# Kernel optimization log

Measured on AMD Instinct MI355X. Metric: run time of the kernel, lower is better.

## Reference

```python
import jax, jax.numpy as jnp
import numpy as np

N = 50000
E = 1600000
DIM = 128
RC = 5.0
DEPTH = 3


def setup_inputs() -> dict:
    key = jax.random.key(0)
    kv, ke, ks, kd, kw, kb, krs, ksig = jax.random.split(key, 8)
    v = jax.random.normal(kv, (N, DIM), dtype=jnp.float32)
    # edge distances in [0, rc]
    e = jax.random.uniform(ke, (E, 1), dtype=jnp.float32) * RC
    src = jax.random.randint(ks, (E,), 0, N, dtype=jnp.int32)
    dst = jax.random.randint(kd, (E,), 0, N, dtype=jnp.int32)
    # learned params: A = nn.Linear(dim, dim); rs, sigma = torch.rand(1)
    A_w = jax.random.normal(kw, (DIM, DIM), dtype=jnp.float32) / np.sqrt(DIM)
    A_b = jax.random.normal(kb, (DIM,), dtype=jnp.float32) * 0.01
    rs = jax.random.uniform(krs, (1,), dtype=jnp.float32)
    sigma = jax.random.uniform(ksig, (1,), dtype=jnp.float32)
    return {"v": v, "e": e, "src": src, "dst": dst,
            "A_w": A_w, "A_b": A_b, "rs": rs, "sigma": sigma}


def _edge_envelope(r, rs, sigma):
    # exp(-(r-rs)^2/sigma^2) * 0.5 * cos(pi*r/rc) * (r < rc)
    gauss = jnp.exp(-jnp.square(r - rs) / jnp.square(sigma))
    cutoff = 0.5 * jnp.cos(np.pi * r / RC) * (r < RC).astype(r.dtype)
    return gauss * cutoff


def reference(v, e, src, dst, A_w, A_b, rs, sigma):
    f = _edge_envelope(e, rs, sigma)  # [E, 1]
    cur = v
    for _ in range(DEPTH):
        msg = f * cur[src]  # gather src node feats, weight by edge envelope: [E, DIM]
        svf = jax.ops.segment_sum(msg, dst, num_segments=N)  # scatter-sum to dst: [N, DIM]
        cur = jax.nn.relu((svf + v) @ A_w.T + A_b)  # linear + relu, skip from original v
    return cur
```

## Files before the change

### kernel.cpp

```cpp
#include <hip/hip_runtime.h>
#include <math.h>

#define N_NODES 50000
#define N_PAD   50048
#define N_EDGES 1600000
#define DIM     128
#define RCUT    5.0f
#define NGROUP  (N_PAD / 64)
#define NB_PRE  512
#define CH_PRE  (N_EDGES / NB_PRE)
#define NB_CONV 6250
#define NB_WPREP 8
#define NB_SUB  8
#define B_SUB   (NB_PRE / NB_SUB)
#define XPAD    136
#define NTILE   (N_PAD / 16)

typedef __attribute__((ext_vector_type(8))) __bf16 bf16x8;
typedef __attribute__((ext_vector_type(4))) float  f32x4;

__device__ __forceinline__ float bf_lo(unsigned int u) { return __uint_as_float(u << 16); }
__device__ __forceinline__ float bf_hi(unsigned int u) { return __uint_as_float(u & 0xffff0000u); }
__device__ __forceinline__ unsigned short f2bf(float x) {
    unsigned int u = __float_as_uint(x);
    u += 0x7fffu + ((u >> 16) & 1u);
    return (unsigned short)(u >> 16);
}

__global__ __launch_bounds__(256) void preA_kernel(
        const float* __restrict__ v, unsigned short* __restrict__ vb,
        const float* __restrict__ Aw, uint4* __restrict__ wfrag,
        const int* __restrict__ dst, int* __restrict__ partial) {
    int b = blockIdx.x;
    if (b < NB_CONV) {
        int i = b * 256 + threadIdx.x;
        float4 x = ((const float4*)v)[i];
        uint2 o;
        o.x = (unsigned)f2bf(x.x) | ((unsigned)f2bf(x.y) << 16);
        o.y = (unsigned)f2bf(x.z) | ((unsigned)f2bf(x.w) << 16);
        ((uint2*)vb)[i] = o;
    } else if (b < NB_CONV + NB_WPREP) {
        int t = (b - NB_CONV) * 256 + threadIdx.x;
        int lane = t & 63, nt = (t >> 6) & 7, kk = t >> 9;
        int n  = nt * 16 + (lane & 15);
        int k0 = kk * 32 + (lane >> 4) * 8;
        unsigned short h[8];
        #pragma unroll
        for (int i = 0; i < 8; ++i) h[i] = f2bf(Aw[n * DIM + k0 + i]);
        uint4 o;
        o.x = h[0] | ((unsigned)h[1] << 16); o.y = h[2] | ((unsigned)h[3] << 16);
        o.z = h[4] | ((unsigned)h[5] << 16); o.w = h[6] | ((unsigned)h[7] << 16);
        wfrag[t] = o;
    } else {
        __shared__ int h[NGROUP];
        int cb = b - NB_CONV - NB_WPREP, tid = threadIdx.x;
        for (int g = tid; g < NGROUP; g += 256) h[g] = 0;
        __syncthreads();
        int beg = cb * CH_PRE, end = beg + CH_PRE;
        for (int i = beg + tid; i < end; i += 256)
            atomicAdd(&h[dst[i] >> 6], 1);
        __syncthreads();
        for (int g = tid; g < NGROUP; g += 256) partial[cb * NGROUP + g] = h[g];
    }
}

__global__ __launch_bounds__(256) void ktot2_kernel(const int* __restrict__ partial,
                                                    int* __restrict__ partial2) {
    int gb = blockIdx.x & 3, bb = blockIdx.x >> 2;
    int g = gb * 256 + threadIdx.x;
    if (g >= NGROUP) return;
    int s = 0;
    int b0 = bb * B_SUB;
    for (int b = b0; b < b0 + B_SUB; ++b) s += partial[b * NGROUP + g];
    partial2[bb * NGROUP + g] = s;
}

__global__ __launch_bounds__(256) void kscan_kernel(const int* __restrict__ partial2,
                                                    int* __restrict__ goff) {
    __shared__ int part[256];
    int tid = threadIdx.x;
    int i0 = tid * 4;
    int v[4]; int s = 0;
    #pragma unroll
    for (int k = 0; k < 4; ++k) {
        int i = i0 + k; int t = 0;
        if (i < NGROUP) {
            #pragma unroll
            for (int bb = 0; bb < NB_SUB; ++bb) t += partial2[bb * NGROUP + i];
        }
        v[k] = t; s += t;
    }
    part[tid] = s; __syncthreads();
    for (int d = 1; d < 256; d <<= 1) {
        int val = (tid >= d) ? part[tid - d] : 0;
        __syncthreads(); part[tid] += val; __syncthreads();
    }
    int run = (tid == 0) ? 0 : part[tid - 1];
    #pragma unroll
    for (int k = 0; k < 4; ++k) {
        int i = i0 + k;
        if (i < NGROUP) { goff[i] = run; run += v[k]; }
    }
    if (tid == 0) goff[NGROUP] = N_EDGES;
}

__global__ __launch_bounds__(256) void kbase2_kernel(const int* __restrict__ partial,
                                                     const int* __restrict__ partial2,
                                                     const int* __restrict__ goff,
                                                     int* __restrict__ pbase) {
    int gb = blockIdx.x & 3, bb = blockIdx.x >> 2;
    int g = gb * 256 + threadIdx.x;
    if (g >= NGROUP) return;
    int run = goff[g];
    for (int b2 = 0; b2 < bb; ++b2) run += partial2[b2 * NGROUP + g];
    int b0 = bb * B_SUB;
    for (int b = b0; b < b0 + B_SUB; ++b) {
        pbase[b * NGROUP + g] = run;
        run += partial[b * NGROUP + g];
    }
}

__global__ __launch_bounds__(512) void reorder_kernel(
        const float* __restrict__ e,
        const int*   __restrict__ src,
        const int*   __restrict__ dst,
        const float* __restrict__ rs,
        const float* __restrict__ sigma,
        const int*   __restrict__ pbase,
        int2* __restrict__ metaT) {
    __shared__ int base[NGROUP];
    __shared__ int cnt[NGROUP];
    int b = blockIdx.x, tid = threadIdx.x;
    for (int g = tid; g < NGROUP; g += 512) { base[g] = pbase[b * NGROUP + g]; cnt[g] = 0; }
    __syncthreads();
    float rsv = rs[0], sg = sigma[0];
    int beg = b * CH_PRE, end = beg + CH_PRE;
    for (int i = beg + tid; i < end; i += 512) {
        float r  = e[i];
        float d  = r - rsv;
        float gauss = expf(-(d * d) / (sg * sg));
        float cut   = 0.5f * cosf(r * (float)(M_PI / (double)RCUT));
        cut = (r < RCUT) ? cut : 0.0f;
        float fe = gauss * cut;
        int dn = dst[i];
        int g  = dn >> 6;
        int lr = atomicAdd(&cnt[g], 1);
        metaT[base[g] + lr] = make_int2(src[i] * (DIM * 2) | ((dn & 63) << 24),
                                        __float_as_int(fe));
    }
}

#define EDGE2(mx, mf, rr)                                        \
    do {                                                         \
        float ff = __int_as_float(mf);                           \
        a0 = fmaf(ff, bf_lo(rr), a0);                            \
        a1 = fmaf(ff, bf_hi(rr), a1);                            \
    } while (0)

__device__ __forceinline__ void gather_node(
        const int2* __restrict__ meta, const char* basec,
        int beg, int end, float& a0, float& a1) {
    int c = beg;
    if ((c & 1) && c < end) {
        int2 m = meta[c];
        unsigned rr = *(const unsigned*)(basec + (unsigned)m.x);
        EDGE2(m.x, m.y, rr);
        ++c;
    }
    for (; c + 16 <= end; c += 16) {
        int4 m0 = *(const int4*)(meta + c);
        int4 m1 = *(const int4*)(meta + c + 2);
        int4 m2 = *(const int4*)(meta + c + 4);
        int4 m3 = *(const int4*)(meta + c + 6);
        int4 m4 = *(const int4*)(meta + c + 8);
        int4 m5 = *(const int4*)(meta + c + 10);
        int4 m6 = *(const int4*)(meta + c + 12);
        int4 m7 = *(const int4*)(meta + c + 14);
        unsigned r0  = *(const unsigned*)(basec + (unsigned)m0.x);
        unsigned r1  = *(const unsigned*)(basec + (unsigned)m0.z);
        unsigned r2  = *(const unsigned*)(basec + (unsigned)m1.x);
        unsigned r3  = *(const unsigned*)(basec + (unsigned)m1.z);
        unsigned r4  = *(const unsigned*)(basec + (unsigned)m2.x);
        unsigned r5  = *(const unsigned*)(basec + (unsigned)m2.z);
        unsigned r6  = *(const unsigned*)(basec + (unsigned)m3.x);
        unsigned r7  = *(const unsigned*)(basec + (unsigned)m3.z);
        unsigned r8  = *(const unsigned*)(basec + (unsigned)m4.x);
        unsigned r9  = *(const unsigned*)(basec + (unsigned)m4.z);
        unsigned r10 = *(const unsigned*)(basec + (unsigned)m5.x);
        unsigned r11 = *(const unsigned*)(basec + (unsigned)m5.z);
        unsigned r12 = *(const unsigned*)(basec + (unsigned)m6.x);
        unsigned r13 = *(const unsigned*)(basec + (unsigned)m6.z);
        unsigned r14 = *(const unsigned*)(basec + (unsigned)m7.x);
        unsigned r15 = *(const unsigned*)(basec + (unsigned)m7.z);
        EDGE2(m0.x, m0.y, r0);  EDGE2(m0.z, m0.w, r1);
        EDGE2(m1.x, m1.y, r2);  EDGE2(m1.z, m1.w, r3);
        EDGE2(m2.x, m2.y, r4);  EDGE2(m2.z, m2.w, r5);
        EDGE2(m3.x, m3.y, r6);  EDGE2(m3.z, m3.w, r7);
        EDGE2(m4.x, m4.y, r8);  EDGE2(m4.z, m4.w, r9);
        EDGE2(m5.x, m5.y, r10); EDGE2(m5.z, m5.w, r11);
        EDGE2(m6.x, m6.y, r12); EDGE2(m6.z, m6.w, r13);
        EDGE2(m7.x, m7.y, r14); EDGE2(m7.z, m7.w, r15);
    }
    if (c + 8 <= end) {
        int4 m0 = *(const int4*)(meta + c);
        int4 m1 = *(const int4*)(meta + c + 2);
        int4 m2 = *(const int4*)(meta + c + 4);
        int4 m3 = *(const int4*)(meta + c + 6);
        unsigned r0 = *(const unsigned*)(basec + (unsigned)m0.x);
        unsigned r1 = *(const unsigned*)(basec + (unsigned)m0.z);
        unsigned r2 = *(const unsigned*)(basec + (unsigned)m1.x);
        unsigned r3 = *(const unsigned*)(basec + (unsigned)m1.z);
        unsigned r4 = *(const unsigned*)(basec + (unsigned)m2.x);
        unsigned r5 = *(const unsigned*)(basec + (unsigned)m2.z);
        unsigned r6 = *(const unsigned*)(basec + (unsigned)m3.x);
        unsigned r7 = *(const unsigned*)(basec + (unsigned)m3.z);
        EDGE2(m0.x, m0.y, r0); EDGE2(m0.z, m0.w, r1);
        EDGE2(m1.x, m1.y, r2); EDGE2(m1.z, m1.w, r3);
        EDGE2(m2.x, m2.y, r4); EDGE2(m2.z, m2.w, r5);
        EDGE2(m3.x, m3.y, r6); EDGE2(m3.z, m3.w, r7);
        c += 8;
    }
    for (; c < end; ++c) {
        int2 m = meta[c];
        unsigned rr = *(const unsigned*)(basec + (unsigned)m.x);
        EDGE2(m.x, m.y, rr);
    }
}

__global__ __launch_bounds__(512) void layer0_kernel(
        const unsigned short* __restrict__ cur,
        const unsigned short* __restrict__ vb,
        const int2*  __restrict__ metaT,
        const int*   __restrict__ goff,
        int2* __restrict__ meta,
        int*  __restrict__ off,
        const uint4* __restrict__ wfrag,
        const float* __restrict__ bias,
        unsigned short* __restrict__ out_bf) {
    __shared__ unsigned short xlds[64 * XPAD];
    __shared__ int c64[64], b64[65], cu64[64];
    int tid = threadIdx.x;
    int wv  = tid >> 6, lane = tid & 63;
    int g   = blockIdx.x;
    int sbeg = goff[g], send = goff[g + 1];

    if (tid < 64) c64[tid] = 0;
    __syncthreads();
    for (int i = sbeg + tid; i < send; i += 512)
        atomicAdd(&c64[(metaT[i].x >> 24) & 63], 1);
    __syncthreads();
    if (tid == 0) {
        int run = 0;
        #pragma unroll
        for (int t = 0; t < 64; ++t) { b64[t] = run; cu64[t] = run; run += c64[t]; }
        b64[64] = run;
    }
    __syncthreads();
    if (tid < 64) {
        int node = g * 64 + tid;
        if (node <= N_NODES) off[node] = sbeg + b64[tid];
    }
    for (int i = sbeg + tid; i < send; i += 512) {
        int2 m = metaT[i];
        int tag = (m.x >> 24) & 63;
        int lr = atomicAdd(&cu64[tag], 1);
        meta[sbeg + lr] = make_int2(m.x & 0x00FFFFFF, m.y);
    }
    __syncthreads();

    int n0 = g * 64 + wv * 8;
    int myoff = 0;
    if (lane < 9) myoff = sbeg + b64[wv * 8 + lane];
    const char* basec = (const char*)cur + lane * 4;

    #pragma unroll 1
    for (int q = 0; q < 8; ++q) {
        int nl = wv * 8 + q;
        int n  = n0 + q;
        float a0 = 0.f, a1 = 0.f;
        if (n < N_NODES) {
            unsigned vv = *(const unsigned*)((const char*)vb + (size_t)n * (DIM * 2) + lane * 4);
            a0 = bf_lo(vv); a1 = bf_hi(vv);
            int beg = __builtin_amdgcn_readlane(myoff, q);
            int end = __builtin_amdgcn_readlane(myoff, q + 1);
            gather_node(meta, basec, beg, end, a0, a1);
        }
        *(unsigned*)(xlds + nl * XPAD + lane * 2) =
            (unsigned)f2bf(a0) | ((unsigned)f2bf(a1) << 16);
    }
    __syncthreads();

    int quad = lane >> 4, l16 = lane & 15;
    int rb = wv >> 1, nh = wv & 1;
    f32x4 acc[4];
    #pragma unroll
    for (int j = 0; j < 4; ++j) acc[j] = (f32x4){0.f, 0.f, 0.f, 0.f};

    const unsigned short* xp = xlds + (rb * 16 + l16) * XPAD + quad * 8;
    #pragma unroll
    for (int kk = 0; kk < 4; ++kk) {
        bf16x8 af = *(const bf16x8*)(xp + kk * 32);
        #pragma unroll
        for (int j = 0; j < 4; ++j) {
            uint4 w = wfrag[(kk * 8 + nh * 4 + j) * 64 + lane];
            bf16x8 bfr = __builtin_bit_cast(bf16x8, w);
            acc[j] = __builtin_amdgcn_mfma_f32_16x16x32_bf16(af, bfr, acc[j], 0, 0, 0);
        }
    }

    int orow0 = g * 64 + rb * 16 + quad * 4;
    #pragma unroll
    for (int j = 0; j < 4; ++j) {
        int col = (nh * 4 + j) * 16 + l16;
        float b = bias[col];
        #pragma unroll
        for (int r = 0; r < 4; ++r) {
            int orow = orow0 + r;
            if (orow < N_NODES)
                out_bf[(size_t)orow * DIM + col] = f2bf(fmaxf(acc[j][r] + b, 0.f));
        }
    }
}

__global__ __launch_bounds__(128, 8) void layer12_kernel(
        const unsigned short* __restrict__ cur,
        const unsigned short* __restrict__ vb,
        const int2*  __restrict__ meta,
        const int*   __restrict__ off,
        const uint4* __restrict__ wfrag,
        const float* __restrict__ bias,
        unsigned short* __restrict__ out_bf,
        float* __restrict__ out_f,
        int last) {
    __shared__ unsigned short xlds[16 * XPAD];
    int tid = threadIdx.x;
    int wv  = tid >> 6, lane = tid & 63;
    int tile = blockIdx.x;
    int n0  = tile * 16 + wv * 8;

    int offidx = n0 + ((lane < 9) ? lane : 8);
    if (offidx > N_NODES) offidx = N_NODES;
    int myoff = off[offidx];
    const char* basec = (const char*)cur + lane * 4;

    #pragma unroll 1
    for (int q = 0; q < 8; ++q) {
        int nl = wv * 8 + q;
        int n  = n0 + q;
        float a0 = 0.f, a1 = 0.f;
        if (n < N_NODES) {
            unsigned vv = *(const unsigned*)((const char*)vb + (size_t)n * (DIM * 2) + lane * 4);
            a0 = bf_lo(vv); a1 = bf_hi(vv);
            int beg = __builtin_amdgcn_readlane(myoff, q);
            int end = __builtin_amdgcn_readlane(myoff, q + 1);
            gather_node(meta, basec, beg, end, a0, a1);
        }
        *(unsigned*)(xlds + nl * XPAD + lane * 2) =
            (unsigned)f2bf(a0) | ((unsigned)f2bf(a1) << 16);
    }
    __syncthreads();

    int quad = lane >> 4, l16 = lane & 15;
    f32x4 acc[4];
    #pragma unroll
    for (int j = 0; j < 4; ++j) acc[j] = (f32x4){0.f, 0.f, 0.f, 0.f};

    const unsigned short* xp = xlds + l16 * XPAD + quad * 8;
    #pragma unroll
    for (int kk = 0; kk < 4; ++kk) {
        bf16x8 af = *(const bf16x8*)(xp + kk * 32);
        #pragma unroll
        for (int j = 0; j < 4; ++j) {
            uint4 w = wfrag[(kk * 8 + wv * 4 + j) * 64 + lane];
            bf16x8 bfr = __builtin_bit_cast(bf16x8, w);
            acc[j] = __builtin_amdgcn_mfma_f32_16x16x32_bf16(af, bfr, acc[j], 0, 0, 0);
        }
    }

    int orow0 = tile * 16 + quad * 4;
    #pragma unroll
    for (int j = 0; j < 4; ++j) {
        int col = (wv * 4 + j) * 16 + l16;
        float b = bias[col];
        #pragma unroll
        for (int r = 0; r < 4; ++r) {
            int orow = orow0 + r;
            if (orow < N_NODES) {
                float val = fmaxf(acc[j][r] + b, 0.f);
                if (last) out_f[(size_t)orow * DIM + col] = val;
                else      out_bf[(size_t)orow * DIM + col] = f2bf(val);
            }
        }
    }
}

extern "C" void kernel_launch(void* const* d_in, const int* in_sizes, int n_in,
                              void* d_out, int out_size, void* d_ws, size_t ws_size,
                              hipStream_t stream) {
    const float* v     = (const float*)d_in[0];
    const float* e     = (const float*)d_in[1];
    const int*   src   = (const int*)  d_in[2];
    const int*   dst   = (const int*)  d_in[3];
    const float* Aw    = (const float*)d_in[4];
    const float* Ab    = (const float*)d_in[5];
    const float* rs    = (const float*)d_in[6];
    const float* sigma = (const float*)d_in[7];
    float* out = (float*)d_out;

    char* p = (char*)d_ws;
    int2*           meta  = (int2*)p;            p += (size_t)N_EDGES * 8;
    unsigned short* bufV  = (unsigned short*)p;  p += (size_t)N_PAD * DIM * 2;
    unsigned short* bufA  = (unsigned short*)p;  p += (size_t)N_PAD * DIM * 2;
    unsigned short* bufB  = (unsigned short*)p;  p += (size_t)N_PAD * DIM * 2;
    uint4*          wfrag = (uint4*)p;           p += 2048 * 16;
    int*            off   = (int*)p;             p += (size_t)(N_NODES + 1) * 4;
    int*            goff  = (int*)p;             p += (NGROUP + 2) * 4;
    int2* metaT    = (int2*)bufA;
    int*  partial  = (int*)bufB;
    int*  pbase    = partial + NB_PRE * NGROUP;
    int*  partial2 = pbase + NB_PRE * NGROUP;

    preA_kernel<<<NB_CONV + NB_WPREP + NB_PRE, 256, 0, stream>>>(
        v, bufV, Aw, wfrag, dst, partial);
    ktot2_kernel<<<4 * NB_SUB, 256, 0, stream>>>(partial, partial2);
    kscan_kernel<<<1, 256, 0, stream>>>(partial2, goff);
    kbase2_kernel<<<4 * NB_SUB, 256, 0, stream>>>(partial, partial2, goff, pbase);
    reorder_kernel<<<NB_PRE, 512, 0, stream>>>(e, src, dst, rs, sigma, pbase, metaT);

    layer0_kernel<<<NGROUP, 512, 0, stream>>>(
        bufV, bufV, metaT, goff, meta, off, wfrag, Ab, bufB);
    layer12_kernel<<<NTILE, 128, 0, stream>>>(
        bufB, bufV, meta, off, wfrag, Ab, bufA, nullptr, 0);
    layer12_kernel<<<NTILE, 128, 0, stream>>>(
        bufA, bufV, meta, off, wfrag, Ab, nullptr, out, 1);
}
```

Measured before the change: 332.7 us.

## Fuse group-offset scan into reorder kernel and coarsen reorder blocks

Replaces the separate partial-sum, scan and per-block-base kernels with one transpose/reduce kernel. The global scan and per-block base computation move into the reorder kernel, which each block repeats redundantly. Reorder now uses 128 blocks covering four histogram chunks each. The aim is to cut launch overhead and serial dependencies in preprocessing. The cost is redundant scan work per block and fewer reorder blocks to fill the GPU.

Measured after the change: 346.9 us. +4.3%, slower.

```diff
diff --git a/kernel.cpp b/kernel.cpp
--- a/kernel.cpp
+++ b/kernel.cpp
@@ -11,8 +11,8 @@
 #define CH_PRE  (N_EDGES / NB_PRE)
 #define NB_CONV 6250
 #define NB_WPREP 8
-#define NB_SUB  8
-#define B_SUB   (NB_PRE / NB_SUB)
+#define NB_RE   128
+#define CH_RE   (N_EDGES / NB_RE)
 #define XPAD    136
 #define NTILE   (N_PAD / 16)
 
@@ -64,60 +64,26 @@
     }
 }
 
-__global__ __launch_bounds__(256) void ktot2_kernel(const int* __restrict__ partial,
-                                                    int* __restrict__ partial2) {
-    int gb = blockIdx.x & 3, bb = blockIdx.x >> 2;
+__global__ __launch_bounds__(256) void ktot2t_kernel(const int* __restrict__ partial,
+                                                     int* __restrict__ partial4T,
+                                                     int* __restrict__ sum64T) {
+    int gb = blockIdx.x & 3, qq = blockIdx.x >> 2;
     int g = gb * 256 + threadIdx.x;
     if (g >= NGROUP) return;
-    int s = 0;
-    int b0 = bb * B_SUB;
-    for (int b = b0; b < b0 + B_SUB; ++b) s += partial[b * NGROUP + g];
-    partial2[bb * NGROUP + g] = s;
-}
-
-__global__ __launch_bounds__(256) void kscan_kernel(const int* __restrict__ partial2,
-                                                    int* __restrict__ goff) {
-    __shared__ int part[256];
-    int tid = threadIdx.x;
-    int i0 = tid * 4;
-    int v[4]; int s = 0;
-    #pragma unroll
-    for (int k = 0; k < 4; ++k) {
-        int i = i0 + k; int t = 0;
-        if (i < NGROUP) {
-            #pragma unroll
-            for (int bb = 0; bb < NB_SUB; ++bb) t += partial2[bb * NGROUP + i];
-        }
-        v[k] = t; s += t;
-    }
-    part[tid] = s; __syncthreads();
-    for (int d = 1; d < 256; d <<= 1) {
-        int val = (tid >= d) ? part[tid - d] : 0;
-        __syncthreads(); part[tid] += val; __syncthreads();
-    }
-    int run = (tid == 0) ? 0 : part[tid - 1];
-    #pragma unroll
-    for (int k = 0; k < 4; ++k) {
-        int i = i0 + k;
-        if (i < NGROUP) { goff[i] = run; run += v[k]; }
-    }
-    if (tid == 0) goff[NGROUP] = N_EDGES;
-}
-
-__global__ __launch_bounds__(256) void kbase2_kernel(const int* __restrict__ partial,
-                                                     const int* __restrict__ partial2,
-                                                     const int* __restrict__ goff,
-                                                     int* __restrict__ pbase) {
-    int gb = blockIdx.x & 3, bb = blockIdx.x >> 2;
-    int g = gb * 256 + threadIdx.x;
-    if (g >= NGROUP) return;
-    int run = goff[g];
-    for (int b2 = 0; b2 < bb; ++b2) run += partial2[b2 * NGROUP + g];
-    int b0 = bb * B_SUB;
-    for (int b = b0; b < b0 + B_SUB; ++b) {
-        pbase[b * NGROUP + g] = run;
-        run += partial[b * NGROUP + g];
-    }
+    int acc = 0;
+    int loc[16];
+    #pragma unroll 1
+    for (int j = 0; j < 16; ++j) {
+        int s4 = 0;
+        #pragma unroll
+        for (int c = 0; c < 4; ++c)
+            s4 += partial[(qq * 64 + j * 4 + c) * NGROUP + g];
+        loc[j] = s4;
+        acc += s4;
+    }
+    #pragma unroll
+    for (int j = 0; j < 16; ++j) partial4T[g * 128 + qq * 16 + j] = loc[j];
+    sum64T[g * 8 + qq] = acc;
 }
 
 __global__ __launch_bounds__(512) void reorder_kernel(
@@ -126,15 +92,49 @@
         const int*   __restrict__ dst,
         const float* __restrict__ rs,
         const float* __restrict__ sigma,
-        const int*   __restrict__ pbase,
+        const int*   __restrict__ partial4T,
+        const int*   __restrict__ sum64T,
+        int*  __restrict__ goff,
         int2* __restrict__ metaT) {
     __shared__ int base[NGROUP];
     __shared__ int cnt[NGROUP];
+    __shared__ int part[512];
     int b = blockIdx.x, tid = threadIdx.x;
-    for (int g = tid; g < NGROUP; g += 512) { base[g] = pbase[b * NGROUP + g]; cnt[g] = 0; }
+    int i0 = tid * 2;
+    int v0 = 0, v1 = 0;
+    if (i0 < NGROUP) {
+        #pragma unroll
+        for (int qq = 0; qq < 8; ++qq) v0 += sum64T[i0 * 8 + qq];
+    }
+    if (i0 + 1 < NGROUP) {
+        #pragma unroll
+        for (int qq = 0; qq < 8; ++qq) v1 += sum64T[(i0 + 1) * 8 + qq];
+    }
+    part[tid] = v0 + v1; __syncthreads();
+    for (int d = 1; d < 512; d <<= 1) {
+        int val = (tid >= d) ? part[tid - d] : 0;
+        __syncthreads(); part[tid] += val; __syncthreads();
+    }
+    int run = (tid == 0) ? 0 : part[tid - 1];
+    if (i0 < NGROUP) {
+        if (b == 0) goff[i0] = run;
+        int r = run;
+        #pragma unroll 4
+        for (int j = 0; j < b; ++j) r += partial4T[i0 * 128 + j];
+        base[i0] = r; cnt[i0] = 0;
+        int run1 = run + v0;
+        if (i0 + 1 < NGROUP) {
+            if (b == 0) goff[i0 + 1] = run1;
+            int r1 = run1;
+            #pragma unroll 4
+            for (int j = 0; j < b; ++j) r1 += partial4T[(i0 + 1) * 128 + j];
+            base[i0 + 1] = r1; cnt[i0 + 1] = 0;
+        }
+    }
+    if (b == 0 && tid == 0) goff[NGROUP] = N_EDGES;
     __syncthreads();
     float rsv = rs[0], sg = sigma[0];
-    int beg = b * CH_PRE, end = beg + CH_PRE;
+    int beg = b * CH_RE, end = beg + CH_RE;
     for (int i = beg + tid; i < end; i += 512) {
         float r  = e[i];
         float d  = r - rsv;
@@ -413,19 +413,18 @@
     unsigned short* bufA  = (unsigned short*)p;  p += (size_t)N_PAD * DIM * 2;
     unsigned short* bufB  = (unsigned short*)p;  p += (size_t)N_PAD * DIM * 2;
     uint4*          wfrag = (uint4*)p;           p += 2048 * 16;
-    int*            off   = (int*)p;             p += (size_t)(N_NODES + 1) * 4;
+    int*            off   = (int*)p;             p += (size_t)(N_NODES + 2) * 4;
     int*            goff  = (int*)p;             p += (NGROUP + 2) * 4;
-    int2* metaT    = (int2*)bufA;
-    int*  partial  = (int*)bufB;
-    int*  pbase    = partial + NB_PRE * NGROUP;
-    int*  partial2 = pbase + NB_PRE * NGROUP;
+    int2* metaT     = (int2*)bufA;
+    int*  partial   = (int*)bufB;
+    int*  partial4T = partial + NB_PRE * NGROUP;
+    int*  sum64T    = partial4T + NGROUP * 128;
 
     preA_kernel<<<NB_CONV + NB_WPREP + NB_PRE, 256, 0, stream>>>(
         v, bufV, Aw, wfrag, dst, partial);
-    ktot2_kernel<<<4 * NB_SUB, 256, 0, stream>>>(partial, partial2);
-    kscan_kernel<<<1, 256, 0, stream>>>(partial2, goff);
-    kbase2_kernel<<<4 * NB_SUB, 256, 0, stream>>>(partial, partial2, goff, pbase);
-    reorder_kernel<<<NB_PRE, 512, 0, stream>>>(e, src, dst, rs, sigma, pbase, metaT);
+    ktot2t_kernel<<<32, 256, 0, stream>>>(partial, partial4T, sum64T);
+    reorder_kernel<<<NB_RE, 512, 0, stream>>>(
+        e, src, dst, rs, sigma, partial4T, sum64T, goff, metaT);
 
     layer0_kernel<<<NGROUP, 512, 0, stream>>>(
         bufV, bufV, metaT, goff, meta, off, wfrag, Ab, bufB);
```

## Fuse prefix-sum kernels into one grid-synced kernel with software barrier

Applied to the files above, without the earlier changes.

Merges the three small counting/scan/base kernels into one 32-block kernel that uses an atomic-flag global barrier between the column-reduction phase and the scan/base phase. Every block recomputes the group scan redundantly into shared memory, so only one grid sync is needed. This removes two kernel launches and their inter-kernel gaps on the critical path. The cost is spin-waiting and the requirement that all 32 blocks be co-resident, which holds easily on this GPU.

After: 318.3 us. -4.3%, faster.

```diff
diff --git a/kernel.cpp b/kernel.cpp
--- a/kernel.cpp
+++ b/kernel.cpp
@@ -15,6 +15,7 @@
 #define B_SUB   (NB_PRE / NB_SUB)
 #define XPAD    136
 #define NTILE   (N_PAD / 16)
+#define NB_MID  32
 
 typedef __attribute__((ext_vector_type(8))) __bf16 bf16x8;
 typedef __attribute__((ext_vector_type(4))) float  f32x4;
@@ -30,7 +31,8 @@
 __global__ __launch_bounds__(256) void preA_kernel(
         const float* __restrict__ v, unsigned short* __restrict__ vb,
         const float* __restrict__ Aw, uint4* __restrict__ wfrag,
-        const int* __restrict__ dst, int* __restrict__ partial) {
+        const int* __restrict__ dst, int* __restrict__ partial,
+        int* __restrict__ bar) {
     int b = blockIdx.x;
     if (b < NB_CONV) {
         int i = b * 256 + threadIdx.x;
@@ -41,6 +43,8 @@
         ((uint2*)vb)[i] = o;
     } else if (b < NB_CONV + NB_WPREP) {
         int t = (b - NB_CONV) * 256 + threadIdx.x;
+        if (b == NB_CONV && threadIdx.x <= NB_MID)
+            bar[threadIdx.x * 32] = 0;
         int lane = t & 63, nt = (t >> 6) & 7, kk = t >> 9;
         int n  = nt * 16 + (lane & 15);
         int k0 = kk * 32 + (lane >> 4) * 8;
@@ -64,21 +68,56 @@
     }
 }
 
-__global__ __launch_bounds__(256) void ktot2_kernel(const int* __restrict__ partial,
-                                                    int* __restrict__ partial2) {
-    int gb = blockIdx.x & 3, bb = blockIdx.x >> 2;
-    int g = gb * 256 + threadIdx.x;
-    if (g >= NGROUP) return;
-    int s = 0;
-    int b0 = bb * B_SUB;
-    for (int b = b0; b < b0 + B_SUB; ++b) s += partial[b * NGROUP + g];
-    partial2[bb * NGROUP + g] = s;
-}
-
-__global__ __launch_bounds__(256) void kscan_kernel(const int* __restrict__ partial2,
-                                                    int* __restrict__ goff) {
+__device__ __forceinline__ void gsync32(int* bar) {
+    int* rel = bar + NB_MID * 32;
+    __syncthreads();
+    if (threadIdx.x == 0) {
+        __threadfence();
+        __hip_atomic_store(&bar[blockIdx.x * 32], 1,
+                           __ATOMIC_RELAXED, __HIP_MEMORY_SCOPE_AGENT);
+    }
+    if (blockIdx.x == 0) {
+        if (threadIdx.x < NB_MID) {
+            int* cp = &bar[threadIdx.x * 32];
+            while (__hip_atomic_load(cp, __ATOMIC_RELAXED,
+                                     __HIP_MEMORY_SCOPE_AGENT) == 0)
+                __builtin_amdgcn_s_sleep(1);
+        }
+        __syncthreads();
+        if (threadIdx.x == 0) {
+            __threadfence();
+            __hip_atomic_store(rel, 1, __ATOMIC_RELAXED, __HIP_MEMORY_SCOPE_AGENT);
+        }
+    }
+    if (threadIdx.x == 0) {
+        while (__hip_atomic_load(rel, __ATOMIC_RELAXED,
+                                 __HIP_MEMORY_SCOPE_AGENT) == 0)
+            __builtin_amdgcn_s_sleep(1);
+        __threadfence();
+    }
+    __syncthreads();
+}
+
+__global__ __launch_bounds__(256) void kmid_kernel(
+        const int* __restrict__ partial,
+        int* __restrict__ partial2,
+        int* __restrict__ goff,
+        int* __restrict__ pbase,
+        int* __restrict__ bar) {
     __shared__ int part[256];
-    int tid = threadIdx.x;
+    __shared__ int goffL[NGROUP];
+    int tid = threadIdx.x, bid = blockIdx.x;
+    int gb = bid & 3, bb = bid >> 2;
+    int g = gb * 256 + tid;
+
+    if (g < NGROUP) {
+        int s = 0;
+        int b0 = bb * B_SUB;
+        for (int b = b0; b < b0 + B_SUB; ++b) s += partial[b * NGROUP + g];
+        partial2[bb * NGROUP + g] = s;
+    }
+    gsync32(bar);
+
     int i0 = tid * 4;
     int v[4]; int s = 0;
     #pragma unroll
@@ -86,7 +125,7 @@
         int i = i0 + k; int t = 0;
         if (i < NGROUP) {
             #pragma unroll
-            for (int bb = 0; bb < NB_SUB; ++bb) t += partial2[bb * NGROUP + i];
+            for (int b2 = 0; b2 < NB_SUB; ++b2) t += partial2[b2 * NGROUP + i];
         }
         v[k] = t; s += t;
     }
@@ -99,24 +138,23 @@
     #pragma unroll
     for (int k = 0; k < 4; ++k) {
         int i = i0 + k;
-        if (i < NGROUP) { goff[i] = run; run += v[k]; }
-    }
-    if (tid == 0) goff[NGROUP] = N_EDGES;
-}
-
-__global__ __launch_bounds__(256) void kbase2_kernel(const int* __restrict__ partial,
-                                                     const int* __restrict__ partial2,
-                                                     const int* __restrict__ goff,
-                                                     int* __restrict__ pbase) {
-    int gb = blockIdx.x & 3, bb = blockIdx.x >> 2;
-    int g = gb * 256 + threadIdx.x;
-    if (g >= NGROUP) return;
-    int run = goff[g];
-    for (int b2 = 0; b2 < bb; ++b2) run += partial2[b2 * NGROUP + g];
-    int b0 = bb * B_SUB;
-    for (int b = b0; b < b0 + B_SUB; ++b) {
-        pbase[b * NGROUP + g] = run;
-        run += partial[b * NGROUP + g];
+        if (i < NGROUP) {
+            goffL[i] = run;
+            if (bid == 0) goff[i] = run;
+            run += v[k];
+        }
+    }
+    if (bid == 0 && tid == 0) goff[NGROUP] = N_EDGES;
+    __syncthreads();
+
+    if (g < NGROUP) {
+        int r = goffL[g];
+        for (int b2 = 0; b2 < bb; ++b2) r += partial2[b2 * NGROUP + g];
+        int b0 = bb * B_SUB;
+        for (int b = b0; b < b0 + B_SUB; ++b) {
+            pbase[b * NGROUP + g] = r;
+            r += partial[b * NGROUP + g];
+        }
     }
 }
 
@@ -413,18 +451,17 @@
     unsigned short* bufA  = (unsigned short*)p;  p += (size_t)N_PAD * DIM * 2;
     unsigned short* bufB  = (unsigned short*)p;  p += (size_t)N_PAD * DIM * 2;
     uint4*          wfrag = (uint4*)p;           p += 2048 * 16;
-    int*            off   = (int*)p;             p += (size_t)(N_NODES + 1) * 4;
+    int*            off   = (int*)p;             p += (size_t)(N_NODES + 2) * 4;
     int*            goff  = (int*)p;             p += (NGROUP + 2) * 4;
+    int*            bar   = (int*)p;             p += (NB_MID + 1) * 32 * 4;
     int2* metaT    = (int2*)bufA;
     int*  partial  = (int*)bufB;
     int*  pbase    = partial + NB_PRE * NGROUP;
     int*  partial2 = pbase + NB_PRE * NGROUP;
 
     preA_kernel<<<NB_CONV + NB_WPREP + NB_PRE, 256, 0, stream>>>(
-        v, bufV, Aw, wfrag, dst, partial);
-    ktot2_kernel<<<4 * NB_SUB, 256, 0, stream>>>(partial, partial2);
-    kscan_kernel<<<1, 256, 0, stream>>>(partial2, goff);
-    kbase2_kernel<<<4 * NB_SUB, 256, 0, stream>>>(partial, partial2, goff, pbase);
+        v, bufV, Aw, wfrag, dst, partial, bar);
+    kmid_kernel<<<NB_MID, 256, 0, stream>>>(partial, partial2, goff, pbase, bar);
     reorder_kernel<<<NB_PRE, 512, 0, stream>>>(e, src, dst, rs, sigma, pbase, metaT);
 
     layer0_kernel<<<NGROUP, 512, 0, stream>>>(
```
